# Kernel optimization log

Measured on AMD Instinct MI355X. Metric: run time of the kernel, lower is better.

## Reference

```python
import jax, jax.numpy as jnp
import numpy as np

NUM_RADIAL = 6
HIDDEN = 128
OUT_EMB = 256
OUT_CH = 128
NUM_LAYERS = 3
E = 1600000
N_NODES = 50000


def setup_inputs() -> dict:
    key = jax.random.key(0)
    ks = jax.random.split(key, 16)
    inp = {
        "x": jax.random.normal(ks[0], (E, HIDDEN), dtype=jnp.float32),
        "rbf": jax.random.normal(ks[1], (E, NUM_RADIAL), dtype=jnp.float32),
        "idx_i": jax.random.randint(ks[2], (E,), 0, N_NODES, dtype=jnp.int32),
        "num_nodes": N_NODES,
        # torch nn.Linear weights are [out, in]
        "W_basis": jax.random.normal(ks[3], (HIDDEN, NUM_RADIAL), dtype=jnp.float32) * 0.3,
        "W_proj": jax.random.normal(ks[4], (OUT_EMB, HIDDEN), dtype=jnp.float32) * 0.08,
        "W_final": jax.random.normal(ks[5], (OUT_CH, OUT_EMB), dtype=jnp.float32) * 0.06,
    }
    for l in range(NUM_LAYERS):
        inp[f"W{l}"] = jax.random.normal(ks[6 + 2 * l], (OUT_EMB, OUT_EMB), dtype=jnp.float32) * 0.06
        inp[f"b{l}"] = jnp.zeros((OUT_EMB,), dtype=jnp.float32)
    return inp


def reference(x, rbf, idx_i, num_nodes, W_basis, W_proj, W_final, W0, b0, W1, b1, W2, b2):
    # basis_transformation: [E, num_radial] -> [E, hidden]
    basis = rbf @ W_basis.T
    # elementwise mul then edge->node scatter-sum
    msg = basis * x                                  # [E, hidden]
    agg = jax.ops.segment_sum(msg, idx_i, num_segments=num_nodes)  # [N, hidden]
    # output_projection (no bias)
    h = agg @ W_proj.T                                # [N, out_emb]
    for W, b in ((W0, b0), (W1, b1), (W2, b2)):
        h = jax.nn.silu(h @ W.T + b)
    return h @ W_final.T                              # [N, out_channels]
```

## Files before the change

### kernel.cpp

```cpp
#include <hip/hip_runtime.h>

typedef float f4 __attribute__((ext_vector_type(4)));
typedef float f2 __attribute__((ext_vector_type(2)));
typedef short bf16x8 __attribute__((ext_vector_type(8)));
typedef float f32x4 __attribute__((ext_vector_type(4)));

constexpr int HIDDEN     = 128;
constexpr int OUT_EMB    = 256;
constexpr int OUT_CH     = 128;
constexpr int NUM_RADIAL = 6;
constexpr int NBLK       = 64;

__device__ __forceinline__ unsigned short f2bf(float f) {
    unsigned int u = __float_as_uint(f);
    return (unsigned short)((u + 0x7FFFu + ((u >> 16) & 1u)) >> 16);
}
__device__ __forceinline__ float bf2f(unsigned short h) {
    return __uint_as_float(((unsigned int)h) << 16);
}

__global__ __launch_bounds__(256) void zero_kernel(int* __restrict__ p, int n)
{
    int i = blockIdx.x * 256 + threadIdx.x;
    if (i < n) p[i] = 0;
}

__global__ __launch_bounds__(256) void split_kernel(const float* __restrict__ src,
                                                    unsigned short* __restrict__ hi,
                                                    unsigned short* __restrict__ lo, int n)
{
    int i = blockIdx.x * 256 + threadIdx.x;
    if (i < n) {
        float v = src[i];
        unsigned short h = f2bf(v);
        hi[i] = h;
        lo[i] = f2bf(v - bf2f(h));
    }
}

__global__ __launch_bounds__(256) void hist_kernel(const int* __restrict__ idx,
                                                   int* __restrict__ count, long E)
{
    long i = (long)blockIdx.x * blockDim.x + threadIdx.x;
    if (i < E) atomicAdd(&count[idx[i]], 1);
}

__global__ __launch_bounds__(1024) void scan_kernel(const int* __restrict__ count,
                                                    int* __restrict__ start,
                                                    int* __restrict__ cursor, int N)
{
    __shared__ int part[1024];
    const int tid   = threadIdx.x;
    const int chunk = (N + 1023) / 1024;
    const int lo    = tid * chunk;
    const int hi    = min(lo + chunk, N);

    int s = 0;
    for (int i = lo; i < hi; ++i) s += count[i];
    part[tid] = s;
    __syncthreads();

    for (int off = 1; off < 1024; off <<= 1) {
        int v = part[tid];
        int u = (tid >= off) ? part[tid - off] : 0;
        __syncthreads();
        part[tid] = v + u;
        __syncthreads();
    }

    int run = (tid > 0) ? part[tid - 1] : 0;
    for (int i = lo; i < hi; ++i) {
        start[i]  = run;
        cursor[i] = run;
        run += count[i];
    }
    if (tid == 1023) start[N] = part[1023];
}

__global__ __launch_bounds__(256) void scatter_perm_kernel(const int* __restrict__ idx,
                                                           int* __restrict__ cursor,
                                                           int* __restrict__ perm, long E)
{
    long i = (long)blockIdx.x * blockDim.x + threadIdx.x;
    if (i < E) {
        int p = atomicAdd(&cursor[idx[i]], 1);
        perm[p] = (int)i;
    }
}

__device__ __forceinline__ void edge_accum(const float* __restrict__ x,
                                           const float* __restrict__ rbf,
                                           const float wb[4][NUM_RADIAL],
                                           int e, int l, f4& acc)
{
    const float* rp = rbf + (long)e * NUM_RADIAL;
    f2 r01 = *(const f2*)(rp);
    f2 r23 = *(const f2*)(rp + 2);
    f2 r45 = *(const f2*)(rp + 4);
    f4 xv  = *(const f4*)(x + (long)e * HIDDEN + 4 * l);
    float rb[NUM_RADIAL] = {r01[0], r01[1], r23[0], r23[1], r45[0], r45[1]};
#pragma unroll
    for (int c = 0; c < 4; ++c) {
        float b = 0.f;
#pragma unroll
        for (int r = 0; r < NUM_RADIAL; ++r) b = __builtin_fmaf(rb[r], wb[c][r], b);
        acc[c] = __builtin_fmaf(b, xv[c], acc[c]);
    }
}

__global__ __launch_bounds__(256) void gather_kernel(
    const float* __restrict__ x, const float* __restrict__ rbf,
    const float* __restrict__ Wb, const int* __restrict__ perm,
    const int* __restrict__ start, float* __restrict__ agg, int N)
{
    const int lane = threadIdx.x & 63;
    const int half = lane >> 5;
    const int l    = lane & 31;
    const int wid  = threadIdx.x >> 6;
    const int node = blockIdx.x * 4 + wid;
    if (node >= N) return;

    float wb[4][NUM_RADIAL];
#pragma unroll
    for (int c = 0; c < 4; ++c)
#pragma unroll
        for (int r = 0; r < NUM_RADIAL; ++r)
            wb[c][r] = Wb[(4 * l + c) * NUM_RADIAL + r];

    const int j0 = start[node], j1 = start[node + 1];
    f4 acc = {0.f, 0.f, 0.f, 0.f};

    int j = j0 + half;
    for (; j + 2 < j1; j += 4) {
        const int ea = perm[j];
        const int eb = perm[j + 2];
        edge_accum(x, rbf, wb, ea, l, acc);
        edge_accum(x, rbf, wb, eb, l, acc);
    }
    if (j < j1) edge_accum(x, rbf, wb, perm[j], l, acc);

#pragma unroll
    for (int c = 0; c < 4; ++c) acc[c] += __shfl_xor(acc[c], 32);

    if (half == 0)
        *(f4*)(agg + (long)node * HIDDEN + 4 * l) = acc;
}

__device__ __forceinline__ int swz(int node, int col) {
    return (node * 256 + col) ^ ((node & 7) << 3);
}

template <int IN, int OUT, bool BIAS_ACT, bool LAST>
__device__ __forceinline__ void mfma_layer(
    const unsigned short* __restrict__ whi, const unsigned short* __restrict__ wlo,
    const float* __restrict__ bias,
    unsigned short* Hhi, unsigned short* Hlo,
    float* __restrict__ outp, int node0, int N, int w, int lane)
{
    const int lr = lane & 15;
    const int lg = lane >> 4;
    constexpr int NT = OUT / 64;
    const int wbase = w * (OUT / 4);

    f32x4 acc[4][NT];
#pragma unroll
    for (int nt = 0; nt < NT; ++nt) {
        float bb = 0.f;
        if constexpr (BIAS_ACT) bb = bias[wbase + nt * 16 + lr];
#pragma unroll
        for (int mt = 0; mt < 4; ++mt) {
            acc[mt][nt][0] = bb; acc[mt][nt][1] = bb;
            acc[mt][nt][2] = bb; acc[mt][nt][3] = bb;
        }
    }

    for (int ks = 0; ks < IN / 32; ++ks) {
        const int k0 = ks * 32 + lg * 8;
        bf16x8 ah[4], al[4];
#pragma unroll
        for (int mt = 0; mt < 4; ++mt) {
            const int node = mt * 16 + lr;
            const int idx  = swz(node, k0);
            ah[mt] = *(const bf16x8*)&Hhi[idx];
            al[mt] = *(const bf16x8*)&Hlo[idx];
        }
#pragma unroll
        for (int nt = 0; nt < NT; ++nt) {
            const long wrow = (long)(wbase + nt * 16 + lr) * IN + k0;
            bf16x8 bh = *(const bf16x8*)&whi[wrow];
            bf16x8 bl = *(const bf16x8*)&wlo[wrow];
#pragma unroll
            for (int mt = 0; mt < 4; ++mt) {
                acc[mt][nt] = __builtin_amdgcn_mfma_f32_16x16x32_bf16(ah[mt], bh, acc[mt][nt], 0, 0, 0);
                acc[mt][nt] = __builtin_amdgcn_mfma_f32_16x16x32_bf16(al[mt], bh, acc[mt][nt], 0, 0, 0);
                acc[mt][nt] = __builtin_amdgcn_mfma_f32_16x16x32_bf16(ah[mt], bl, acc[mt][nt], 0, 0, 0);
            }
        }
    }

    __syncthreads();

#pragma unroll
    for (int mt = 0; mt < 4; ++mt) {
#pragma unroll
        for (int nt = 0; nt < NT; ++nt) {
#pragma unroll
            for (int r = 0; r < 4; ++r) {
                float v = acc[mt][nt][r];
                if constexpr (BIAS_ACT) v = v / (1.f + __expf(-v));
                const int node = mt * 16 + lg * 4 + r;
                const int col  = wbase + nt * 16 + lr;
                if constexpr (LAST) {
                    if (node0 + node < N) outp[(long)(node0 + node) * OUT + col] = v;
                } else {
                    unsigned short hi = f2bf(v);
                    unsigned short lo = f2bf(v - bf2f(hi));
                    const int idx = swz(node, col);
                    Hhi[idx] = hi;
                    Hlo[idx] = lo;
                }
            }
        }
    }
    if constexpr (!LAST) __syncthreads();
}

__global__ __launch_bounds__(256, 2) void node_mlp_mfma_kernel(
    const float* __restrict__ agg,
    const unsigned short* __restrict__ WpHi, const unsigned short* __restrict__ WpLo,
    const unsigned short* __restrict__ W0Hi, const unsigned short* __restrict__ W0Lo,
    const float* __restrict__ b0,
    const unsigned short* __restrict__ W1Hi, const unsigned short* __restrict__ W1Lo,
    const float* __restrict__ b1,
    const unsigned short* __restrict__ W2Hi, const unsigned short* __restrict__ W2Lo,
    const float* __restrict__ b2,
    const unsigned short* __restrict__ WfHi, const unsigned short* __restrict__ WfLo,
    float* __restrict__ out, int N)
{
    __shared__ unsigned short Hhi[NBLK * 256];
    __shared__ unsigned short Hlo[NBLK * 256];

    const int tid   = threadIdx.x;
    const int w     = tid >> 6;
    const int lane  = tid & 63;
    const int node0 = blockIdx.x * NBLK;

#pragma unroll
    for (int i = 0; i < (NBLK * HIDDEN) / 256; ++i) {
        const int e    = i * 256 + tid;
        const int node = e >> 7;
        const int col  = e & 127;
        float v = 0.f;
        if (node0 + node < N) v = agg[(long)(node0 + node) * HIDDEN + col];
        unsigned short hi = f2bf(v);
        unsigned short lo = f2bf(v - bf2f(hi));
        const int idx = swz(node, col);
        Hhi[idx] = hi;
        Hlo[idx] = lo;
    }
    __syncthreads();

    mfma_layer<HIDDEN,  OUT_EMB, false, false>(WpHi, WpLo, nullptr, Hhi, Hlo, nullptr, node0, N, w, lane);
    mfma_layer<OUT_EMB, OUT_EMB, true,  false>(W0Hi, W0Lo, b0,      Hhi, Hlo, nullptr, node0, N, w, lane);
    mfma_layer<OUT_EMB, OUT_EMB, true,  false>(W1Hi, W1Lo, b1,      Hhi, Hlo, nullptr, node0, N, w, lane);
    mfma_layer<OUT_EMB, OUT_EMB, true,  false>(W2Hi, W2Lo, b2,      Hhi, Hlo, nullptr, node0, N, w, lane);
    mfma_layer<OUT_EMB, OUT_CH,  false, true >(WfHi, WfLo, nullptr, Hhi, Hlo, out,     node0, N, w, lane);
}

extern "C" void kernel_launch(void* const* d_in, const int* in_sizes, int n_in,
                              void* d_out, int out_size, void* d_ws, size_t ws_size,
                              hipStream_t stream)
{
    const float* x   = (const float*)d_in[0];
    const float* rbf = (const float*)d_in[1];
    const int*   idx = (const int*)d_in[2];
    const float* Wb  = (const float*)d_in[4];
    const float* Wp  = (const float*)d_in[5];
    const float* Wf  = (const float*)d_in[6];
    const float* W0  = (const float*)d_in[7];
    const float* b0  = (const float*)d_in[8];
    const float* W1  = (const float*)d_in[9];
    const float* b1  = (const float*)d_in[10];
    const float* W2  = (const float*)d_in[11];
    const float* b2  = (const float*)d_in[12];

    const long E = (long)in_sizes[0] / HIDDEN;
    const int  N = out_size / OUT_CH;

    float* agg    = (float*)d_ws;
    int*   count  = (int*)(agg + (long)N * HIDDEN);
    int*   startp = count + N;
    int*   cursor = startp + N + 1;
    int*   perm   = cursor + N;
    uintptr_t p = (uintptr_t)(perm + E);
    p = (p + 15) & ~(uintptr_t)15;
    unsigned short* WpHi = (unsigned short*)p;
    unsigned short* WpLo = WpHi + 32768;
    unsigned short* W0Hi = WpLo + 32768;
    unsigned short* W0Lo = W0Hi + 65536;
    unsigned short* W1Hi = W0Lo + 65536;
    unsigned short* W1Lo = W1Hi + 65536;
    unsigned short* W2Hi = W1Lo + 65536;
    unsigned short* W2Lo = W2Hi + 65536;
    unsigned short* WfHi = W2Lo + 65536;
    unsigned short* WfLo = WfHi + 32768;

    zero_kernel<<<(N + 255) / 256, 256, 0, stream>>>(count, N);

    split_kernel<<<(32768 + 255) / 256, 256, 0, stream>>>(Wp, WpHi, WpLo, 32768);
    split_kernel<<<(65536 + 255) / 256, 256, 0, stream>>>(W0, W0Hi, W0Lo, 65536);
    split_kernel<<<(65536 + 255) / 256, 256, 0, stream>>>(W1, W1Hi, W1Lo, 65536);
    split_kernel<<<(65536 + 255) / 256, 256, 0, stream>>>(W2, W2Hi, W2Lo, 65536);
    split_kernel<<<(32768 + 255) / 256, 256, 0, stream>>>(Wf, WfHi, WfLo, 32768);

    const int eb = (int)((E + 255) / 256);
    hist_kernel<<<eb, 256, 0, stream>>>(idx, count, E);
    scan_kernel<<<1, 1024, 0, stream>>>(count, startp, cursor, N);
    scatter_perm_kernel<<<eb, 256, 0, stream>>>(idx, cursor, perm, E);
    gather_kernel<<<(N + 3) / 4, 256, 0, stream>>>(x, rbf, Wb, perm, startp, agg, N);

    node_mlp_mfma_kernel<<<(N + NBLK - 1) / NBLK, 256, 0, stream>>>(
        agg, WpHi, WpLo, W0Hi, W0Lo, b0, W1Hi, W1Lo, b1, W2Hi, W2Lo, b2,
        WfHi, WfLo, (float*)d_out, N);
}
```

Before: 710.0 us.

## Drop low-order bf16 split for activations and store agg in bf16

Activations are now kept as single bf16 instead of a hi/lo bf16 pair, so each MLP layer issues two MFMAs per tile instead of three (the weight lo term is kept). The aggregated node features are written by the gather kernel directly as bf16, which halves that buffer's traffic. The smaller shared-memory footprint allows occupancy to be raised to 3 blocks. The zero and five split kernels are merged into one prep launch. Accuracy falls because activation rounding error is no longer compensated.

```diff
diff --git a/kernel.cpp b/kernel.cpp
--- a/kernel.cpp
+++ b/kernel.cpp
@@ -3,6 +3,8 @@
 typedef float f4 __attribute__((ext_vector_type(4)));
 typedef float f2 __attribute__((ext_vector_type(2)));
 typedef short bf16x8 __attribute__((ext_vector_type(8)));
+typedef unsigned short u16x8 __attribute__((ext_vector_type(8)));
+typedef unsigned short u16x4 __attribute__((ext_vector_type(4)));
 typedef float f32x4 __attribute__((ext_vector_type(4)));
 
 constexpr int HIDDEN     = 128;
@@ -11,6 +13,13 @@
 constexpr int NUM_RADIAL = 6;
 constexpr int NBLK       = 64;
 
+constexpr int OFF_Wp = 0;
+constexpr int OFF_W0 = OFF_Wp + 256 * 128;
+constexpr int OFF_W1 = OFF_W0 + 256 * 256;
+constexpr int OFF_W2 = OFF_W1 + 256 * 256;
+constexpr int OFF_Wf = OFF_W2 + 256 * 256;
+constexpr int WTOT   = OFF_Wf + 128 * 256;
+
 __device__ __forceinline__ unsigned short f2bf(float f) {
     unsigned int u = __float_as_uint(f);
     return (unsigned short)((u + 0x7FFFu + ((u >> 16) & 1u)) >> 16);
@@ -19,22 +28,26 @@
     return __uint_as_float(((unsigned int)h) << 16);
 }
 
-__global__ __launch_bounds__(256) void zero_kernel(int* __restrict__ p, int n)
-{
-    int i = blockIdx.x * 256 + threadIdx.x;
-    if (i < n) p[i] = 0;
-}
-
-__global__ __launch_bounds__(256) void split_kernel(const float* __restrict__ src,
-                                                    unsigned short* __restrict__ hi,
-                                                    unsigned short* __restrict__ lo, int n)
-{
-    int i = blockIdx.x * 256 + threadIdx.x;
-    if (i < n) {
-        float v = src[i];
+__global__ __launch_bounds__(256) void prep_kernel(
+    const float* __restrict__ Wp, const float* __restrict__ W0,
+    const float* __restrict__ W1, const float* __restrict__ W2,
+    const float* __restrict__ Wf,
+    unsigned short* __restrict__ whi, unsigned short* __restrict__ wlo,
+    int* __restrict__ count, int N)
+{
+    const int i = blockIdx.x * 256 + threadIdx.x;
+    if (i < N) count[i] = 0;
+    if (i < WTOT) {
+        const float* src; int off;
+        if      (i < OFF_W0) { src = Wp; off = i - OFF_Wp; }
+        else if (i < OFF_W1) { src = W0; off = i - OFF_W0; }
+        else if (i < OFF_W2) { src = W1; off = i - OFF_W1; }
+        else if (i < OFF_Wf) { src = W2; off = i - OFF_W2; }
+        else                 { src = Wf; off = i - OFF_Wf; }
+        float v = src[off];
         unsigned short h = f2bf(v);
-        hi[i] = h;
-        lo[i] = f2bf(v - bf2f(h));
+        whi[i] = h;
+        wlo[i] = f2bf(v - bf2f(h));
     }
 }
 
@@ -111,7 +124,7 @@
 __global__ __launch_bounds__(256) void gather_kernel(
     const float* __restrict__ x, const float* __restrict__ rbf,
     const float* __restrict__ Wb, const int* __restrict__ perm,
-    const int* __restrict__ start, float* __restrict__ agg, int N)
+    const int* __restrict__ start, unsigned short* __restrict__ aggb, int N)
 {
     const int lane = threadIdx.x & 63;
     const int half = lane >> 5;
@@ -142,8 +155,12 @@
 #pragma unroll
     for (int c = 0; c < 4; ++c) acc[c] += __shfl_xor(acc[c], 32);
 
-    if (half == 0)
-        *(f4*)(agg + (long)node * HIDDEN + 4 * l) = acc;
+    if (half == 0) {
+        u16x4 o;
+#pragma unroll
+        for (int c = 0; c < 4; ++c) o[c] = f2bf(acc[c]);
+        *(u16x4*)(aggb + (long)node * HIDDEN + 4 * l) = o;
+    }
 }
 
 __device__ __forceinline__ int swz(int node, int col) {
@@ -154,8 +171,8 @@
 __device__ __forceinline__ void mfma_layer(
     const unsigned short* __restrict__ whi, const unsigned short* __restrict__ wlo,
     const float* __restrict__ bias,
-    unsigned short* Hhi, unsigned short* Hlo,
-    float* __restrict__ outp, int node0, int N, int w, int lane)
+    unsigned short* H, float* __restrict__ outp,
+    int node0, int N, int w, int lane)
 {
     const int lr = lane & 15;
     const int lg = lane >> 4;
@@ -176,13 +193,11 @@
 
     for (int ks = 0; ks < IN / 32; ++ks) {
         const int k0 = ks * 32 + lg * 8;
-        bf16x8 ah[4], al[4];
+        bf16x8 ah[4];
 #pragma unroll
         for (int mt = 0; mt < 4; ++mt) {
             const int node = mt * 16 + lr;
-            const int idx  = swz(node, k0);
-            ah[mt] = *(const bf16x8*)&Hhi[idx];
-            al[mt] = *(const bf16x8*)&Hlo[idx];
+            ah[mt] = *(const bf16x8*)&H[swz(node, k0)];
         }
 #pragma unroll
         for (int nt = 0; nt < NT; ++nt) {
@@ -192,7 +207,6 @@
 #pragma unroll
             for (int mt = 0; mt < 4; ++mt) {
                 acc[mt][nt] = __builtin_amdgcn_mfma_f32_16x16x32_bf16(ah[mt], bh, acc[mt][nt], 0, 0, 0);
-                acc[mt][nt] = __builtin_amdgcn_mfma_f32_16x16x32_bf16(al[mt], bh, acc[mt][nt], 0, 0, 0);
                 acc[mt][nt] = __builtin_amdgcn_mfma_f32_16x16x32_bf16(ah[mt], bl, acc[mt][nt], 0, 0, 0);
             }
         }
@@ -213,11 +227,7 @@
                 if constexpr (LAST) {
                     if (node0 + node < N) outp[(long)(node0 + node) * OUT + col] = v;
                 } else {
-                    unsigned short hi = f2bf(v);
-                    unsigned short lo = f2bf(v - bf2f(hi));
-                    const int idx = swz(node, col);
-                    Hhi[idx] = hi;
-                    Hlo[idx] = lo;
+                    H[swz(node, col)] = f2bf(v);
                 }
             }
         }
@@ -225,20 +235,14 @@
     if constexpr (!LAST) __syncthreads();
 }
 
-__global__ __launch_bounds__(256, 2) void node_mlp_mfma_kernel(
-    const float* __restrict__ agg,
-    const unsigned short* __restrict__ WpHi, const unsigned short* __restrict__ WpLo,
-    const unsigned short* __restrict__ W0Hi, const unsigned short* __restrict__ W0Lo,
-    const float* __restrict__ b0,
-    const unsigned short* __restrict__ W1Hi, const unsigned short* __restrict__ W1Lo,
-    const float* __restrict__ b1,
-    const unsigned short* __restrict__ W2Hi, const unsigned short* __restrict__ W2Lo,
+__global__ __launch_bounds__(256, 3) void node_mlp_mfma_kernel(
+    const unsigned short* __restrict__ aggb,
+    const unsigned short* __restrict__ whi, const unsigned short* __restrict__ wlo,
+    const float* __restrict__ b0, const float* __restrict__ b1,
     const float* __restrict__ b2,
-    const unsigned short* __restrict__ WfHi, const unsigned short* __restrict__ WfLo,
     float* __restrict__ out, int N)
 {
-    __shared__ unsigned short Hhi[NBLK * 256];
-    __shared__ unsigned short Hlo[NBLK * 256];
+    __shared__ unsigned short H[NBLK * 256];
 
     const int tid   = threadIdx.x;
     const int w     = tid >> 6;
@@ -246,25 +250,21 @@
     const int node0 = blockIdx.x * NBLK;
 
 #pragma unroll
-    for (int i = 0; i < (NBLK * HIDDEN) / 256; ++i) {
-        const int e    = i * 256 + tid;
+    for (int i = 0; i < (NBLK * HIDDEN) / (256 * 8); ++i) {
+        const int e    = (i * 256 + tid) * 8;
         const int node = e >> 7;
         const int col  = e & 127;
-        float v = 0.f;
-        if (node0 + node < N) v = agg[(long)(node0 + node) * HIDDEN + col];
-        unsigned short hi = f2bf(v);
-        unsigned short lo = f2bf(v - bf2f(hi));
-        const int idx = swz(node, col);
-        Hhi[idx] = hi;
-        Hlo[idx] = lo;
+        u16x8 v = {0, 0, 0, 0, 0, 0, 0, 0};
+        if (node0 + node < N) v = *(const u16x8*)(aggb + (long)(node0 + node) * HIDDEN + col);
+        *(u16x8*)&H[swz(node, col)] = v;
     }
     __syncthreads();
 
-    mfma_layer<HIDDEN,  OUT_EMB, false, false>(WpHi, WpLo, nullptr, Hhi, Hlo, nullptr, node0, N, w, lane);
-    mfma_layer<OUT_EMB, OUT_EMB, true,  false>(W0Hi, W0Lo, b0,      Hhi, Hlo, nullptr, node0, N, w, lane);
-    mfma_layer<OUT_EMB, OUT_EMB, true,  false>(W1Hi, W1Lo, b1,      Hhi, Hlo, nullptr, node0, N, w, lane);
-    mfma_layer<OUT_EMB, OUT_EMB, true,  false>(W2Hi, W2Lo, b2,      Hhi, Hlo, nullptr, node0, N, w, lane);
-    mfma_layer<OUT_EMB, OUT_CH,  false, true >(WfHi, WfLo, nullptr, Hhi, Hlo, out,     node0, N, w, lane);
+    mfma_layer<HIDDEN,  OUT_EMB, false, false>(whi + OFF_Wp, wlo + OFF_Wp, nullptr, H, nullptr, node0, N, w, lane);
+    mfma_layer<OUT_EMB, OUT_EMB, true,  false>(whi + OFF_W0, wlo + OFF_W0, b0,      H, nullptr, node0, N, w, lane);
+    mfma_layer<OUT_EMB, OUT_EMB, true,  false>(whi + OFF_W1, wlo + OFF_W1, b1,      H, nullptr, node0, N, w, lane);
+    mfma_layer<OUT_EMB, OUT_EMB, true,  false>(whi + OFF_W2, wlo + OFF_W2, b2,      H, nullptr, node0, N, w, lane);
+    mfma_layer<OUT_EMB, OUT_CH,  false, true >(whi + OFF_Wf, wlo + OFF_Wf, nullptr, H, out,     node0, N, w, lane);
 }
 
 extern "C" void kernel_launch(void* const* d_in, const int* in_sizes, int n_in,
@@ -287,39 +287,25 @@
     const long E = (long)in_sizes[0] / HIDDEN;
     const int  N = out_size / OUT_CH;
 
-    float* agg    = (float*)d_ws;
-    int*   count  = (int*)(agg + (long)N * HIDDEN);
-    int*   startp = count + N;
-    int*   cursor = startp + N + 1;
-    int*   perm   = cursor + N;
+    unsigned short* aggb = (unsigned short*)d_ws;
+    int* count  = (int*)(aggb + (long)N * HIDDEN);
+    int* startp = count + N;
+    int* cursor = startp + N + 1;
+    int* perm   = cursor + N;
     uintptr_t p = (uintptr_t)(perm + E);
     p = (p + 15) & ~(uintptr_t)15;
-    unsigned short* WpHi = (unsigned short*)p;
-    unsigned short* WpLo = WpHi + 32768;
-    unsigned short* W0Hi = WpLo + 32768;
-    unsigned short* W0Lo = W0Hi + 65536;
-    unsigned short* W1Hi = W0Lo + 65536;
-    unsigned short* W1Lo = W1Hi + 65536;
-    unsigned short* W2Hi = W1Lo + 65536;
-    unsigned short* W2Lo = W2Hi + 65536;
-    unsigned short* WfHi = W2Lo + 65536;
-    unsigned short* WfLo = WfHi + 32768;
-
-    zero_kernel<<<(N + 255) / 256, 256, 0, stream>>>(count, N);
-
-    split_kernel<<<(32768 + 255) / 256, 256, 0, stream>>>(Wp, WpHi, WpLo, 32768);
-    split_kernel<<<(65536 + 255) / 256, 256, 0, stream>>>(W0, W0Hi, W0Lo, 65536);
-    split_kernel<<<(65536 + 255) / 256, 256, 0, stream>>>(W1, W1Hi, W1Lo, 65536);
-    split_kernel<<<(65536 + 255) / 256, 256, 0, stream>>>(W2, W2Hi, W2Lo, 65536);
-    split_kernel<<<(32768 + 255) / 256, 256, 0, stream>>>(Wf, WfHi, WfLo, 32768);
+    unsigned short* whi = (unsigned short*)p;
+    unsigned short* wlo = whi + WTOT;
+
+    const int pb = (max((int)WTOT, N) + 255) / 256;
+    prep_kernel<<<pb, 256, 0, stream>>>(Wp, W0, W1, W2, Wf, whi, wlo, count, N);
 
     const int eb = (int)((E + 255) / 256);
     hist_kernel<<<eb, 256, 0, stream>>>(idx, count, E);
     scan_kernel<<<1, 1024, 0, stream>>>(count, startp, cursor, N);
     scatter_perm_kernel<<<eb, 256, 0, stream>>>(idx, cursor, perm, E);
-    gather_kernel<<<(N + 3) / 4, 256, 0, stream>>>(x, rbf, Wb, perm, startp, agg, N);
+    gather_kernel<<<(N + 3) / 4, 256, 0, stream>>>(x, rbf, Wb, perm, startp, aggb, N);
 
     node_mlp_mfma_kernel<<<(N + NBLK - 1) / NBLK, 256, 0, stream>>>(
-        agg, WpHi, WpLo, W0Hi, W0Lo, b0, W1Hi, W1Lo, b1, W2Hi, W2Lo, b2,
-        WfHi, WfLo, (float*)d_out, N);
-}
+        aggb, whi, wlo, b0, b1, b2, (float*)d_out, N);
+}
```

Measured after the change: 719.2 us. About the same (+1.3%).
